# Kernel optimization log

Measured on AMD Instinct MI355X. Metric: run time of the kernel, lower is better.

The kernel has to match this reference:

```python
import jax, jax.numpy as jnp
import numpy as np

B, D, H, O, E, TOP_K = 1024, 1024, 2048, 1024, 8, 2


def setup_inputs() -> dict:
    key = jax.random.key(0)
    ks = jax.random.split(key, 8)
    s = 0.02
    return {
        "x":  jax.random.normal(ks[0], (B, D), dtype=jnp.float32),
        "Wr": jax.random.normal(ks[1], (D, E), dtype=jnp.float32) * s,
        "br": jnp.zeros((E,), dtype=jnp.float32),
        "W1": jax.random.normal(ks[2], (E, D, H), dtype=jnp.float32) * s,
        "b1": jnp.zeros((E, H), dtype=jnp.float32),
        "W2": jax.random.normal(ks[3], (E, H, H), dtype=jnp.float32) * s,
        "b2": jnp.zeros((E, H), dtype=jnp.float32),
        "W3": jax.random.normal(ks[4], (E, H, O), dtype=jnp.float32) * s,
        "b3": jnp.zeros((E, O), dtype=jnp.float32),
    }


def reference(x, Wr, br, W1, b1, W2, b2, W3, b3):
    # --- router: softmax -> top-k -> renormalize selected weights ---
    logits = x @ Wr + br                      # [B, E]
    probs = jax.nn.softmax(logits, axis=-1)
    w, ids = jax.lax.top_k(probs, TOP_K)      # [B, K], [B, K]
    w = w / (jnp.sum(w, axis=-1, keepdims=True) + 1e-6)

    # --- expert MLPs (depth=2: in->h, relu, h->h, relu, h->out) ---
    h = jax.nn.relu(jnp.einsum('bd,edh->beh', x, W1) + b1)   # [B, E, H]
    h = jax.nn.relu(jnp.einsum('beh,ehg->beg', h, W2) + b2)  # [B, E, H]
    y_e = jnp.einsum('beg,ego->beo', h, W3) + b3             # [B, E, O]

    # --- weighted scatter-combine: comb[b,e] = sum_k w[b,k] * [ids[b,k]==e] ---
    comb = jnp.sum(jax.nn.one_hot(ids, E, dtype=x.dtype) * w[..., None], axis=1)  # [B, E]
    out = jnp.einsum('beo,be->bo', y_e, comb)                # [B, O]
    return out
```

## Files before the change

kernel.cpp:

```cpp
#include <hip/hip_runtime.h>
#include <hip/hip_bf16.h>

#define BT 1024
#define DD 1024
#define HH 2048
#define OO 1024
#define EE 8
#define RMAX 3072

typedef __bf16 bf16x8 __attribute__((ext_vector_type(8)));
typedef float  f32x4  __attribute__((ext_vector_type(4)));

__device__ __forceinline__ void cp16(void* l, const void* g) {
    __builtin_amdgcn_global_load_lds(
        (const __attribute__((address_space(1))) void*)g,
        (__attribute__((address_space(3))) void*)l, 16, 0, 0);
}

#define VMW(n)  asm volatile("s_waitcnt vmcnt(" #n ")" ::: "memory")
#define LGKM(n) asm volatile("s_waitcnt lgkmcnt(" #n ")" ::: "memory")
#define SCHED0  __builtin_amdgcn_sched_barrier(0)
#define BAR()   __builtin_amdgcn_s_barrier()


__global__ __launch_bounds__(256) void router_kernel(
    const float* __restrict__ x, const float* __restrict__ Wr, const float* __restrict__ br,
    int* __restrict__ counts, int* __restrict__ elist,
    int* __restrict__ tok_e, int* __restrict__ tok_p, float* __restrict__ tok_w)
{
    int b = blockIdx.x;
    int tid = threadIdx.x;
    float acc[EE];
#pragma unroll
    for (int e = 0; e < EE; ++e) acc[e] = 0.f;
    const float* xr = x + (size_t)b * DD;
    for (int d = tid; d < DD; d += 256) {
        float xv = xr[d];
#pragma unroll
        for (int e = 0; e < EE; ++e) acc[e] += xv * Wr[d * EE + e];
    }
    __shared__ float red[4][EE];
    int lane = tid & 63, wv = tid >> 6;
#pragma unroll
    for (int e = 0; e < EE; ++e) {
        float v = acc[e];
#pragma unroll
        for (int o = 32; o > 0; o >>= 1) v += __shfl_down(v, o, 64);
        if (lane == 0) red[wv][e] = v;
    }
    __syncthreads();
    if (tid == 0) {
        float lg[EE];
#pragma unroll
        for (int e = 0; e < EE; ++e) lg[e] = red[0][e] + red[1][e] + red[2][e] + red[3][e] + br[e];
        float mx = lg[0];
#pragma unroll
        for (int e = 1; e < EE; ++e) mx = fmaxf(mx, lg[e]);
        float s = 0.f, p[EE];
#pragma unroll
        for (int e = 0; e < EE; ++e) { p[e] = expf(lg[e] - mx); s += p[e]; }
        float inv = 1.f / s;
#pragma unroll
        for (int e = 0; e < EE; ++e) p[e] *= inv;
        int i0 = 0; float b0 = p[0];
#pragma unroll
        for (int e = 1; e < EE; ++e) if (p[e] > b0) { b0 = p[e]; i0 = e; }
        int i1 = -1; float b1v = -1.f;
#pragma unroll
        for (int e = 0; e < EE; ++e) if (e != i0 && p[e] > b1v) { b1v = p[e]; i1 = e; }
        float s2 = b0 + b1v + 1e-6f;
        float w0 = b0 / s2, w1 = b1v / s2;
        int p0 = atomicAdd(&counts[i0], 1);
        int p1 = atomicAdd(&counts[i1], 1);
        elist[i0 * 1024 + p0] = b;
        elist[i1 * 1024 + p1] = b;
        tok_e[2 * b] = i0; tok_e[2 * b + 1] = i1;
        tok_p[2 * b] = p0; tok_p[2 * b + 1] = p1;
        tok_w[2 * b] = w0; tok_w[2 * b + 1] = w1;
    }
}

__global__ void offsets_kernel(const int* __restrict__ counts, int* __restrict__ off)
{
    if (threadIdx.x == 0 && blockIdx.x == 0) {
        int a = 0;
        for (int e = 0; e < EE; ++e) {
            off[e] = a;
            a += ((counts[e] + 127) >> 7) << 7;
        }
        off[EE] = a;
    }
}

__global__ __launch_bounds__(256) void gather_kernel(
    const float* __restrict__ x, const int* __restrict__ counts, const int* __restrict__ off,
    const int* __restrict__ elist, __bf16* __restrict__ Xg)
{
    int e = blockIdx.y;
    int chunk = blockIdx.x >> 2;
    int rg = blockIdx.x & 3;
    int cnt = counts[e];
    if (chunk * 128 >= cnt) return;
    int base = off[e] + chunk * 128 + rg * 32;
    int tid = threadIdx.x;
    for (int it = 0; it < 32; ++it) {
        int slot = chunk * 128 + rg * 32 + it;
        __bf16 v[4];
        if (slot < cnt) {
            int tok = elist[e * 1024 + slot];
            const float4 f = *(const float4*)(x + (size_t)tok * DD + tid * 4);
            v[0] = (__bf16)f.x; v[1] = (__bf16)f.y; v[2] = (__bf16)f.z; v[3] = (__bf16)f.w;
        } else {
            v[0] = v[1] = v[2] = v[3] = (__bf16)0.f;
        }
        *(uint2*)(Xg + (size_t)(base + it) * DD + tid * 4) = *(uint2*)v;
    }
}

template <int K, int N, int TN, bool RELU, bool OUT_BF16>
__global__ __launch_bounds__(256, 2) void gemm_fused(
    const __bf16* __restrict__ A, const float* __restrict__ Wall,
    const float* __restrict__ bias, void* __restrict__ OutV,
    const int* __restrict__ counts, const int* __restrict__ off)
{
    constexpr int NSTEPS = K / 64;
    constexpr int NJ  = TN / 32;
    constexpr int BLD = TN / 4;
    constexpr int BSE = TN * 64;

    int e  = blockIdx.x & 7;
    int nt = blockIdx.x >> 3;
    int mt = blockIdx.y;
    int cnt = counts[e];
    if (mt * 128 >= cnt) return;
    int row0 = off[e] + mt * 128;

    const __bf16* Ab = A + (size_t)row0 * K;
    const float*  Wp = Wall + (size_t)e * K * N + nt * TN;

    __shared__ __bf16 As[3 * 8192];
    __shared__ __bf16 Bs[2 * BSE];

    int tid = threadIdx.x;
    int wave = tid >> 6, lane = tid & 63;
    int m = lane & 15, q = lane >> 4;
    int wm = (wave >> 1) * 64, wn = (wave & 1) * (TN / 2);

    int rdma = wave * 8 + (lane >> 3);
    int kxe  = ((lane & 7) ^ (lane >> 3)) * 8;
    int bn  = (TN == 64) ? (tid & 63) : (tid & 31);
    int bkc = (TN == 64) ? ((tid >> 6) * 16) : ((tid >> 5) * 8);
    int c0  = bkc >> 3;
    int bswz = bn & 7;

    float bA[BLD], bB[BLD];
    f32x4 acc[4][NJ] = {};

    auto issueA = [&](int t, unsigned ab) {
#pragma unroll
        for (int i = 0; i < 4; ++i)
            cp16(&As[ab + i * 2048 + wave * 512 + lane * 8],
                 Ab + (size_t)(i * 32 + rdma) * K + t * 64 + kxe);
    };
    auto loadB = [&](int t, float (&br_)[BLD]) {
        const float* p = Wp + (size_t)(t * 64 + bkc) * N + bn;
#pragma unroll
        for (int g = 0; g < BLD; ++g) br_[g] = p[(size_t)g * N];
    };
    auto writeB = [&](unsigned bb, float (&br_)[BLD]) {
        __bf16 t8[BLD];
#pragma unroll
        for (int g = 0; g < BLD; ++g) t8[g] = (__bf16)br_[g];
        *(uint4*)(&Bs[bb + bn * 64 + ((c0    ) ^ bswz) * 8]) = ((const uint4*)t8)[0];
        if constexpr (TN == 64)
            *(uint4*)(&Bs[bb + bn * 64 + ((c0 + 1) ^ bswz) * 8]) = ((const uint4*)t8)[1];
    };

    auto STEP = [&](int t, unsigned aR, unsigned aW, unsigned bR, unsigned bW,
                    float (&bWr)[BLD], float (&bLd)[BLD]) {
        BAR(); SCHED0;
        bool pf = (t + 2 < NSTEPS);
        if (pf) { issueA(t + 2, aW); loadB(t + 2, bLd); }
        bf16x8 af[4][2], bfr[NJ][2];
#pragma unroll
        for (int kk = 0; kk < 2; ++kk) {
#pragma unroll
            for (int i = 0; i < 4; ++i)
                af[i][kk] = *(bf16x8*)(&As[aR + (wm + i * 16 + m) * 64 + (((kk * 4 + q) ^ (m & 7)) * 8)]);
#pragma unroll
            for (int j = 0; j < NJ; ++j)
                bfr[j][kk] = *(bf16x8*)(&Bs[bR + (wn + j * 16 + m) * 64 + (((kk * 4 + q) ^ (m & 7)) * 8)]);
        }
        if constexpr (NJ == 2) LGKM(6); else LGKM(5);
        SCHED0;
        __builtin_amdgcn_s_setprio(1);
#pragma unroll
        for (int i = 0; i < 4; ++i)
#pragma unroll
            for (int j = 0; j < NJ; ++j)
                acc[i][j] = __builtin_amdgcn_mfma_f32_16x16x32_bf16(af[i][0], bfr[j][0], acc[i][j], 0, 0, 0);
        LGKM(0); SCHED0;
#pragma unroll
        for (int i = 0; i < 4; ++i)
#pragma unroll
            for (int j = 0; j < NJ; ++j)
                acc[i][j] = __builtin_amdgcn_mfma_f32_16x16x32_bf16(af[i][1], bfr[j][1], acc[i][j], 0, 0, 0);
        __builtin_amdgcn_s_setprio(0);
        if (t + 1 < NSTEPS) {
            if (pf) { if constexpr (TN == 64) VMW(20); else VMW(12); }
            else    { VMW(0); }
            SCHED0;
            writeB(bW, bWr);
            LGKM(0);
        }
    };

    issueA(0, 0u);
    issueA(1, 8192u);
    loadB(0, bA);
    loadB(1, bB);
    if constexpr (TN == 64) VMW(16); else VMW(8);
    SCHED0;
    writeB(0u, bA);
    LGKM(0);

    unsigned aR = 0u, aM = 8192u, aW = 16384u;
    for (int t = 0; t < NSTEPS; t += 2) {
        STEP(t,     aR, aW, 0u,            (unsigned)BSE, bB, bA);
        { unsigned tp = aR; aR = aM; aM = aW; aW = tp; }
        STEP(t + 1, aR, aW, (unsigned)BSE, 0u,            bA, bB);
        { unsigned tp = aR; aR = aM; aM = aW; aW = tp; }
    }

    const float* bp = bias + (size_t)e * N;
    int colbase = nt * TN + wn;
#pragma unroll
    for (int j = 0; j < NJ; ++j) {
        int col = colbase + j * 16 + m;
        float bv = bp[col];
#pragma unroll
        for (int i = 0; i < 4; ++i) {
            int rbase = row0 + wm + i * 16 + q * 4;
#pragma unroll
            for (int r = 0; r < 4; ++r) {
                float v = acc[i][j][r] + bv;
                if constexpr (RELU) v = fmaxf(v, 0.f);
                if constexpr (OUT_BF16)
                    ((__bf16*)OutV)[(size_t)(rbase + r) * N + col] = (__bf16)v;
                else
                    ((float*)OutV)[(size_t)(rbase + r) * N + col] = v;
            }
        }
    }
}

__global__ __launch_bounds__(256) void combine_kernel(
    const float* __restrict__ Y, const int* __restrict__ off,
    const int* __restrict__ tok_e, const int* __restrict__ tok_p,
    const float* __restrict__ tok_w, float* __restrict__ out)
{
    int b = blockIdx.x, t = threadIdx.x;
    int e0 = tok_e[2 * b], e1 = tok_e[2 * b + 1];
    int r0 = off[e0] + tok_p[2 * b];
    int r1 = off[e1] + tok_p[2 * b + 1];
    float w0 = tok_w[2 * b], w1 = tok_w[2 * b + 1];
    int col = t * 4;
    f32x4 s0 = *(const f32x4*)(Y + (size_t)r0 * OO + col);
    f32x4 s1 = *(const f32x4*)(Y + (size_t)r1 * OO + col);
    f32x4 o = s0 * w0 + s1 * w1;
    *(f32x4*)(out + (size_t)b * OO + col) = o;
}

extern "C" void kernel_launch(void* const* d_in, const int* in_sizes, int n_in,
                              void* d_out, int out_size, void* d_ws, size_t ws_size,
                              hipStream_t stream)
{
    (void)in_sizes; (void)n_in; (void)out_size; (void)ws_size;
    const float* x  = (const float*)d_in[0];
    const float* Wr = (const float*)d_in[1];
    const float* br = (const float*)d_in[2];
    const float* W1 = (const float*)d_in[3];
    const float* b1 = (const float*)d_in[4];
    const float* W2 = (const float*)d_in[5];
    const float* b2 = (const float*)d_in[6];
    const float* W3 = (const float*)d_in[7];
    const float* b3 = (const float*)d_in[8];
    float* out = (float*)d_out;

    char* ws = (char*)d_ws;
    int*    counts = (int*)(ws + 0);
    int*    off    = (int*)(ws + 256);
    int*    tok_e  = (int*)(ws + 1024);
    int*    tok_p  = (int*)(ws + 9216);
    float*  tok_w  = (float*)(ws + 17408);
    int*    elist  = (int*)(ws + 25600);
    __bf16* Xg     = (__bf16*)(ws + 65536);
    __bf16* H1     = (__bf16*)(ws + 6356992);
    __bf16* H2     = (__bf16*)(ws + 18939904);
    float*  Y      = (float*)(ws + 31522816);

    hipMemsetAsync(counts, 0, 256, stream);
    router_kernel<<<1024, 256, 0, stream>>>(x, Wr, br, counts, elist, tok_e, tok_p, tok_w);
    offsets_kernel<<<1, 64, 0, stream>>>(counts, off);
    gather_kernel<<<dim3(32, 8), 256, 0, stream>>>(x, counts, off, elist, Xg);

    gemm_fused<1024, 2048, 64, true,  true ><<<dim3(256, 8), 256, 0, stream>>>(Xg, W1, b1, (void*)H1, counts, off);
    gemm_fused<2048, 2048, 64, true,  true ><<<dim3(256, 8), 256, 0, stream>>>(H1, W2, b2, (void*)H2, counts, off);
    gemm_fused<2048, 1024, 32, false, false><<<dim3(256, 8), 256, 0, stream>>>(H2, W3, b3, (void*)Y,  counts, off);

    combine_kernel<<<1024, 256, 0, stream>>>(Y, off, tok_e, tok_p, tok_w, out);
}
```

Baseline: 433.0 us.

## Pre-convert expert weights to pre-tiled swizzled bf16 and DMA B tiles to LDS

Adds a wprep kernel that converts each expert's fp32 weights to bf16 once per call, storing them in a 64x64 tile-contiguous, pre-swizzled layout. The GEMMs can then fetch B tiles with direct global-to-LDS async copies in a triple-buffered pipeline, instead of strided fp32 register loads followed by conversion and LDS writes. The third GEMM moves to 64-wide N tiles, which halves its grid. The cost is an extra read of the fp32 weights plus a bf16 write and re-read on every call.

```diff
diff --git a/kernel.cpp b/kernel.cpp
--- a/kernel.cpp
+++ b/kernel.cpp
@@ -117,16 +117,55 @@
     }
 }
 
-template <int K, int N, int TN, bool RELU, bool OUT_BF16>
+template <int K, int N>
+__global__ __launch_bounds__(256) void wprep(const float* __restrict__ W, __bf16* __restrict__ Wb)
+{
+    constexpr int NSL = N / 512;
+    int ks = blockIdx.x, e = blockIdx.y;
+    int t = threadIdx.x;
+    const float* Wp = W + (size_t)e * K * N + (size_t)ks * 64 * N;
+    __shared__ __bf16 T[512 * 72];
+
+    for (int s = 0; s < NSL; ++s) {
+#pragma unroll
+        for (int i = 0; i < 4; ++i) {
+            int tau = i * 256 + t;
+            int nti = tau & 127;
+            int kt  = tau >> 7;
+            float4 f[8];
+#pragma unroll
+            for (int rr = 0; rr < 8; ++rr)
+                f[rr] = *(const float4*)(Wp + (size_t)(kt * 8 + rr) * N + s * 512 + nti * 4);
+#pragma unroll
+            for (int j = 0; j < 4; ++j) {
+                __bf16 t8[8];
+#pragma unroll
+                for (int rr = 0; rr < 8; ++rr) t8[rr] = (__bf16)((&f[rr].x)[j]);
+                *(uint4*)(&T[(nti * 4 + j) * 72 + kt * 8]) = *(uint4*)t8;
+            }
+        }
+        __syncthreads();
+#pragma unroll
+        for (int i = 0; i < 16; ++i) {
+            int idx = i * 256 + t;
+            int ntg = idx >> 9;
+            int rem = idx & 511;
+            int n = rem >> 3, c = rem & 7;
+            uint4 v = *(const uint4*)(&T[(ntg * 64 + n) * 72 + (c ^ (n & 7)) * 8]);
+            size_t dst = ((((size_t)e * (N / 64) + (s * 8 + ntg)) * (K / 64) + ks) << 12) + (size_t)rem * 8;
+            *(uint4*)(&Wb[dst]) = v;
+        }
+        __syncthreads();
+    }
+}
+
+template <int K, int N, bool RELU, bool OUT_BF16>
 __global__ __launch_bounds__(256, 2) void gemm_fused(
-    const __bf16* __restrict__ A, const float* __restrict__ Wall,
+    const __bf16* __restrict__ A, const __bf16* __restrict__ Wb,
     const float* __restrict__ bias, void* __restrict__ OutV,
     const int* __restrict__ counts, const int* __restrict__ off)
 {
     constexpr int NSTEPS = K / 64;
-    constexpr int NJ  = TN / 32;
-    constexpr int BLD = TN / 4;
-    constexpr int BSE = TN * 64;
 
     int e  = blockIdx.x & 7;
     int nt = blockIdx.x >> 3;
@@ -136,106 +175,80 @@
     int row0 = off[e] + mt * 128;
 
     const __bf16* Ab = A + (size_t)row0 * K;
-    const float*  Wp = Wall + (size_t)e * K * N + nt * TN;
+    const __bf16* Bp = Wb + ((size_t)e * (N / 64) + nt) * (size_t)(K / 64) * 4096;
 
     __shared__ __bf16 As[3 * 8192];
-    __shared__ __bf16 Bs[2 * BSE];
+    __shared__ __bf16 Bs[3 * 4096];
 
     int tid = threadIdx.x;
     int wave = tid >> 6, lane = tid & 63;
     int m = lane & 15, q = lane >> 4;
-    int wm = (wave >> 1) * 64, wn = (wave & 1) * (TN / 2);
+    int wm = (wave >> 1) * 64, wn = (wave & 1) * 32;
 
     int rdma = wave * 8 + (lane >> 3);
     int kxe  = ((lane & 7) ^ (lane >> 3)) * 8;
-    int bn  = (TN == 64) ? (tid & 63) : (tid & 31);
-    int bkc = (TN == 64) ? ((tid >> 6) * 16) : ((tid >> 5) * 8);
-    int c0  = bkc >> 3;
-    int bswz = bn & 7;
-
-    float bA[BLD], bB[BLD];
-    f32x4 acc[4][NJ] = {};
-
-    auto issueA = [&](int t, unsigned ab) {
+
+    f32x4 acc[4][2] = {};
+
+    auto issue = [&](int t) {
+        unsigned ab = (unsigned)(t % 3) * 8192;
+        unsigned bb = (unsigned)(t % 3) * 4096;
 #pragma unroll
         for (int i = 0; i < 4; ++i)
             cp16(&As[ab + i * 2048 + wave * 512 + lane * 8],
                  Ab + (size_t)(i * 32 + rdma) * K + t * 64 + kxe);
+#pragma unroll
+        for (int r = 0; r < 2; ++r)
+            cp16(&Bs[bb + r * 2048 + wave * 512 + lane * 8],
+                 Bp + (size_t)t * 4096 + r * 2048 + wave * 512 + lane * 8);
     };
-    auto loadB = [&](int t, float (&br_)[BLD]) {
-        const float* p = Wp + (size_t)(t * 64 + bkc) * N + bn;
-#pragma unroll
-        for (int g = 0; g < BLD; ++g) br_[g] = p[(size_t)g * N];
-    };
-    auto writeB = [&](unsigned bb, float (&br_)[BLD]) {
-        __bf16 t8[BLD];
-#pragma unroll
-        for (int g = 0; g < BLD; ++g) t8[g] = (__bf16)br_[g];
-        *(uint4*)(&Bs[bb + bn * 64 + ((c0    ) ^ bswz) * 8]) = ((const uint4*)t8)[0];
-        if constexpr (TN == 64)
-            *(uint4*)(&Bs[bb + bn * 64 + ((c0 + 1) ^ bswz) * 8]) = ((const uint4*)t8)[1];
-    };
-
-    auto STEP = [&](int t, unsigned aR, unsigned aW, unsigned bR, unsigned bW,
-                    float (&bWr)[BLD], float (&bLd)[BLD]) {
-        BAR(); SCHED0;
-        bool pf = (t + 2 < NSTEPS);
-        if (pf) { issueA(t + 2, aW); loadB(t + 2, bLd); }
-        bf16x8 af[4][2], bfr[NJ][2];
-#pragma unroll
-        for (int kk = 0; kk < 2; ++kk) {
-#pragma unroll
-            for (int i = 0; i < 4; ++i)
-                af[i][kk] = *(bf16x8*)(&As[aR + (wm + i * 16 + m) * 64 + (((kk * 4 + q) ^ (m & 7)) * 8)]);
-#pragma unroll
-            for (int j = 0; j < NJ; ++j)
-                bfr[j][kk] = *(bf16x8*)(&Bs[bR + (wn + j * 16 + m) * 64 + (((kk * 4 + q) ^ (m & 7)) * 8)]);
-        }
-        if constexpr (NJ == 2) LGKM(6); else LGKM(5);
+
+    issue(0);
+    issue(1);
+
+    for (int t = 0; t < NSTEPS; ++t) {
+        if (t == NSTEPS - 1) { VMW(0); } else { VMW(6); }
         SCHED0;
+        BAR();
+        SCHED0;
+        if (t + 2 < NSTEPS) issue(t + 2);
+
+        unsigned aR = (unsigned)(t % 3) * 8192;
+        unsigned bR = (unsigned)(t % 3) * 4096;
+        bf16x8 af0[4], bf0[2], af1[4], bf1[2];
+#pragma unroll
+        for (int i = 0; i < 4; ++i)
+            af0[i] = *(bf16x8*)(&As[aR + (wm + i * 16 + m) * 64 + ((q) ^ (m & 7)) * 8]);
+#pragma unroll
+        for (int j = 0; j < 2; ++j)
+            bf0[j] = *(bf16x8*)(&Bs[bR + (wn + j * 16 + m) * 64 + ((q) ^ (m & 7)) * 8]);
+        SCHED0;
+#pragma unroll
+        for (int i = 0; i < 4; ++i)
+            af1[i] = *(bf16x8*)(&As[aR + (wm + i * 16 + m) * 64 + ((4 + q) ^ (m & 7)) * 8]);
+#pragma unroll
+        for (int j = 0; j < 2; ++j)
+            bf1[j] = *(bf16x8*)(&Bs[bR + (wn + j * 16 + m) * 64 + ((4 + q) ^ (m & 7)) * 8]);
+        LGKM(6); SCHED0;
         __builtin_amdgcn_s_setprio(1);
 #pragma unroll
         for (int i = 0; i < 4; ++i)
 #pragma unroll
-            for (int j = 0; j < NJ; ++j)
-                acc[i][j] = __builtin_amdgcn_mfma_f32_16x16x32_bf16(af[i][0], bfr[j][0], acc[i][j], 0, 0, 0);
+            for (int j = 0; j < 2; ++j)
+                acc[i][j] = __builtin_amdgcn_mfma_f32_16x16x32_bf16(af0[i], bf0[j], acc[i][j], 0, 0, 0);
         LGKM(0); SCHED0;
 #pragma unroll
         for (int i = 0; i < 4; ++i)
 #pragma unroll
-            for (int j = 0; j < NJ; ++j)
-                acc[i][j] = __builtin_amdgcn_mfma_f32_16x16x32_bf16(af[i][1], bfr[j][1], acc[i][j], 0, 0, 0);
+            for (int j = 0; j < 2; ++j)
+                acc[i][j] = __builtin_amdgcn_mfma_f32_16x16x32_bf16(af1[i], bf1[j], acc[i][j], 0, 0, 0);
         __builtin_amdgcn_s_setprio(0);
-        if (t + 1 < NSTEPS) {
-            if (pf) { if constexpr (TN == 64) VMW(20); else VMW(12); }
-            else    { VMW(0); }
-            SCHED0;
-            writeB(bW, bWr);
-            LGKM(0);
-        }
-    };
-
-    issueA(0, 0u);
-    issueA(1, 8192u);
-    loadB(0, bA);
-    loadB(1, bB);
-    if constexpr (TN == 64) VMW(16); else VMW(8);
-    SCHED0;
-    writeB(0u, bA);
-    LGKM(0);
-
-    unsigned aR = 0u, aM = 8192u, aW = 16384u;
-    for (int t = 0; t < NSTEPS; t += 2) {
-        STEP(t,     aR, aW, 0u,            (unsigned)BSE, bB, bA);
-        { unsigned tp = aR; aR = aM; aM = aW; aW = tp; }
-        STEP(t + 1, aR, aW, (unsigned)BSE, 0u,            bA, bB);
-        { unsigned tp = aR; aR = aM; aM = aW; aW = tp; }
     }
 
     const float* bp = bias + (size_t)e * N;
-    int colbase = nt * TN + wn;
-#pragma unroll
-    for (int j = 0; j < NJ; ++j) {
+    int colbase = nt * 64 + wn;
+#pragma unroll
+    for (int j = 0; j < 2; ++j) {
         int col = colbase + j * 16 + m;
         float bv = bp[col];
 #pragma unroll
@@ -298,15 +311,22 @@
     __bf16* H1     = (__bf16*)(ws + 6356992);
     __bf16* H2     = (__bf16*)(ws + 18939904);
     float*  Y      = (float*)(ws + 31522816);
+    __bf16* Wb1    = (__bf16*)(ws + 44105728);
+    __bf16* Wb2    = (__bf16*)(ws + 77660160);
+    __bf16* Wb3    = (__bf16*)(ws + 144769024);
 
     hipMemsetAsync(counts, 0, 256, stream);
     router_kernel<<<1024, 256, 0, stream>>>(x, Wr, br, counts, elist, tok_e, tok_p, tok_w);
     offsets_kernel<<<1, 64, 0, stream>>>(counts, off);
     gather_kernel<<<dim3(32, 8), 256, 0, stream>>>(x, counts, off, elist, Xg);
 
-    gemm_fused<1024, 2048, 64, true,  true ><<<dim3(256, 8), 256, 0, stream>>>(Xg, W1, b1, (void*)H1, counts, off);
-    gemm_fused<2048, 2048, 64, true,  true ><<<dim3(256, 8), 256, 0, stream>>>(H1, W2, b2, (void*)H2, counts, off);
-    gemm_fused<2048, 1024, 32, false, false><<<dim3(256, 8), 256, 0, stream>>>(H2, W3, b3, (void*)Y,  counts, off);
+    wprep<1024, 2048><<<dim3(16, 8), 256, 0, stream>>>(W1, Wb1);
+    wprep<2048, 2048><<<dim3(32, 8), 256, 0, stream>>>(W2, Wb2);
+    wprep<2048, 1024><<<dim3(32, 8), 256, 0, stream>>>(W3, Wb3);
+
+    gemm_fused<1024, 2048, true,  true ><<<dim3(256, 8), 256, 0, stream>>>(Xg, Wb1, b1, (void*)H1, counts, off);
+    gemm_fused<2048, 2048, true,  true ><<<dim3(256, 8), 256, 0, stream>>>(H1, Wb2, b2, (void*)H2, counts, off);
+    gemm_fused<2048, 1024, false, false><<<dim3(128, 8), 256, 0, stream>>>(H2, Wb3, b3, (void*)Y,  counts, off);
 
     combine_kernel<<<1024, 256, 0, stream>>>(Y, off, tok_e, tok_p, tok_w, out);
 }
```

Measured after the change: 496.4 us. 1.15x slower.
